# Optimization experiments

Hardware: AMD Instinct MI355X
Metric: run time of the kernel (lower is better)

## Reference

```python
import jax, jax.numpy as jnp
import numpy as np

LN_EPS = 1e-5
B, N, D, V = 2048, 8, 1024, 4096


def setup_inputs() -> dict:
    key = jax.random.key(0)
    k1, k2, k3, k4 = jax.random.split(key, 4)
    return {
        "input_embedding": jax.random.normal(k1, (B, D), dtype=jnp.float32),
        "features": jax.random.randint(k2, (B, N), 0, V, dtype=jnp.int64),
        "embed_tables": jax.random.normal(k3, (N, V, D), dtype=jnp.float32) * 0.02,
        "W_pred": jax.random.normal(k4, (N, D, V), dtype=jnp.float32) * 0.02,
        "b_pred": jnp.zeros((N, V), dtype=jnp.float32),
        "ln_gamma": jnp.ones((D,), dtype=jnp.float32),
        "ln_beta": jnp.zeros((D,), dtype=jnp.float32),
    }


def reference(input_embedding, features, embed_tables, W_pred, b_pred, ln_gamma, ln_beta):
    # Per-feature embedding lookup: embed_tables[n, features[b,n]] -> [B, N, D]
    feat_emb = embed_tables[jnp.arange(N)[None, :], features]
    # Stack input embedding in front: [B, N+1, D]
    embeddings = jnp.concatenate([input_embedding[:, None, :], feat_emb], axis=1)
    # Original: triu(diag=1) mask-multiply-sum then [:, 1:, :].
    # masked_sums[:, t] = sum_{s < t} emb[:, s]; slicing t=1..N == inclusive cumsum
    # over the first N positions.
    masked_sums = jnp.cumsum(embeddings, axis=1)[:, :-1, :]  # [B, N, D]
    # LayerNorm over last dim
    mu = jnp.mean(masked_sums, axis=-1, keepdims=True)
    var = jnp.var(masked_sums, axis=-1, keepdims=True)
    h = (masked_sums - mu) / jnp.sqrt(var + LN_EPS) * ln_gamma + ln_beta
    # Exact (erf) GELU, matching nn.GELU default
    h = jax.nn.gelu(h, approximate=False)
    # Per-feature predictor heads as one batched GEMM: [B, N, V]
    logits = jnp.einsum("bnd,ndv->bnv", h, W_pred) + b_pred
    return logits
```

## Files before the change

### kernel.cpp

```cpp
#include <hip/hip_runtime.h>
#include <hip/hip_bf16.h>

#define B_ 2048
#define N_ 8
#define D_ 1024
#define V_ 4096
#define LN_EPS_ 1e-5f

typedef __bf16 bf16x8 __attribute__((ext_vector_type(8)));
typedef float f32x4 __attribute__((ext_vector_type(4)));

#define GLB(p) ((const __attribute__((address_space(1))) void*)(p))
#define LDSP(p) ((__attribute__((address_space(3))) void*)(p))

static __device__ __forceinline__ unsigned short f2bf(float x) {
    union { float f; unsigned int u; } v;
    v.f = x;
    unsigned int r = v.u + 0x7fffu + ((v.u >> 16) & 1u);
    return (unsigned short)(r >> 16);
}

__global__ __launch_bounds__(256) void prep(const float* __restrict__ ie,
                                            const int* __restrict__ feats,
                                            const float* __restrict__ emb,
                                            const float* __restrict__ gamma,
                                            const float* __restrict__ beta,
                                            const float* __restrict__ W,
                                            unsigned short* __restrict__ H,
                                            unsigned short* __restrict__ Wt) {
    const int bid = blockIdx.x;
    const int t = threadIdx.x;

    if (bid >= 2048) {
        __shared__ unsigned short tile[64][65];
        const int w  = bid - 2048;
        const int v0 = (w & 63) * 64;
        const int d0 = ((w >> 6) & 15) * 64;
        const int n  = w >> 10;
        const int tx = t & 15, ty = t >> 4;
#pragma unroll
        for (int i = 0; i < 4; ++i) {
            const int d = ty + i * 16;
            const float4 w4 = *(const float4*)&W[((size_t)n * D_ + d0 + d) * V_ + v0 + tx * 4];
            tile[d][tx * 4 + 0] = f2bf(w4.x);
            tile[d][tx * 4 + 1] = f2bf(w4.y);
            tile[d][tx * 4 + 2] = f2bf(w4.z);
            tile[d][tx * 4 + 3] = f2bf(w4.w);
        }
        __syncthreads();
#pragma unroll
        for (int i = 0; i < 4; ++i) {
            const int v = ty + i * 16;
            ushort4 pk;
            pk.x = tile[tx * 4 + 0][v];
            pk.y = tile[tx * 4 + 1][v];
            pk.z = tile[tx * 4 + 2][v];
            pk.w = tile[tx * 4 + 3][v];
            *reinterpret_cast<ushort4*>(&Wt[((size_t)n * V_ + v0 + v) * D_ + d0 + tx * 4]) = pk;
        }
    } else {
        __shared__ float redS[4], redQ[4];
        const int b = bid;
        const int d0 = t * 4;
        const int lane = t & 63, wid = t >> 6;

        float4 s  = *(const float4*)&ie[(size_t)b * D_ + d0];
        const float4 g4 = *(const float4*)&gamma[d0];
        const float4 be4 = *(const float4*)&beta[d0];

        int fc[N_];
#pragma unroll
        for (int n = 0; n < N_; ++n) fc[n] = feats[b * N_ + n];

#pragma unroll
        for (int n = 0; n < N_; ++n) {
            float ls = s.x + s.y + s.z + s.w;
            float lq = s.x * s.x + s.y * s.y + s.z * s.z + s.w * s.w;
#pragma unroll
            for (int off = 32; off > 0; off >>= 1) {
                ls += __shfl_down(ls, off, 64);
                lq += __shfl_down(lq, off, 64);
            }
            if (lane == 0) { redS[wid] = ls; redQ[wid] = lq; }
            __syncthreads();
            const float tot  = redS[0] + redS[1] + redS[2] + redS[3];
            const float totq = redQ[0] + redQ[1] + redQ[2] + redQ[3];
            __syncthreads();

            const float mu   = tot * (1.0f / D_);
            const float var  = totq * (1.0f / D_) - mu * mu;
            const float rstd = rsqrtf(var + LN_EPS_);

            float h0 = (s.x - mu) * rstd * g4.x + be4.x;
            float h1 = (s.y - mu) * rstd * g4.y + be4.y;
            float h2 = (s.z - mu) * rstd * g4.z + be4.z;
            float h3 = (s.w - mu) * rstd * g4.w + be4.w;
            h0 = 0.5f * h0 * (1.0f + erff(h0 * 0.70710678f));
            h1 = 0.5f * h1 * (1.0f + erff(h1 * 0.70710678f));
            h2 = 0.5f * h2 * (1.0f + erff(h2 * 0.70710678f));
            h3 = 0.5f * h3 * (1.0f + erff(h3 * 0.70710678f));

            ushort4 pk;
            pk.x = f2bf(h0); pk.y = f2bf(h1); pk.z = f2bf(h2); pk.w = f2bf(h3);
            *reinterpret_cast<ushort4*>(&H[((size_t)n * B_ + b) * D_ + d0]) = pk;

            const float4 e = *(const float4*)&emb[((size_t)n * V_ + fc[n]) * (size_t)D_ + d0];
            s.x += e.x; s.y += e.y; s.z += e.z; s.w += e.w;
        }
    }
}

#define MF(a, b, c) __builtin_amdgcn_mfma_f32_16x16x32_bf16((a), (b), (c), 0, 0, 0)

#define STAGE(As, Bs, bb) { \
    __builtin_amdgcn_global_load_lds(GLB((As) + (size_t)srow * D_ + gsl),         LDSP(lds + (bb) + t * 16), 16, 0, 0); \
    __builtin_amdgcn_global_load_lds(GLB((As) + (size_t)(srow + 128) * D_ + gsl), LDSP(lds + (bb) + 8192 + t * 16), 16, 0, 0); \
    __builtin_amdgcn_global_load_lds(GLB((Bs) + (size_t)srow * D_ + gsl),         LDSP(lds + (bb) + 16384 + t * 16), 16, 0, 0); \
    __builtin_amdgcn_global_load_lds(GLB((Bs) + (size_t)(srow + 128) * D_ + gsl), LDSP(lds + (bb) + 24576 + t * 16), 16, 0, 0); \
}

#define RD_A(i, bb) (*(const bf16x8*)(lds + (bb) + ((i) * 32 + wr * 16 + lrow) * 64 + swk))
#define RD_B(j, bb) (*(const bf16x8*)(lds + (bb) + 16384 + (wc * 64 + (j) * 16 + lrow) * 64 + swk))

#define TILE1(bc, bn, As, Bs) { \
    asm volatile("s_waitcnt vmcnt(8)" ::: "memory"); \
    __builtin_amdgcn_s_barrier(); \
    STAGE(As, Bs, bn); \
    bf16x8 Bf[4], Af[4]; \
    _Pragma("unroll") for (int j = 0; j < 4; ++j) Bf[j] = RD_B(j, bc); \
    _Pragma("unroll") for (int i = 0; i < 4; ++i) Af[i] = RD_A(i, bc); \
    __builtin_amdgcn_s_setprio(1); \
    _Pragma("unroll") for (int i = 0; i < 4; ++i) \
        _Pragma("unroll") for (int j = 0; j < 4; ++j) \
            acc[i][j] = MF(Af[i], Bf[j], acc[i][j]); \
    __builtin_amdgcn_s_setprio(0); \
    _Pragma("unroll") for (int i = 0; i < 4; ++i) Af[i] = RD_A((i) + 4, bc); \
    __builtin_amdgcn_s_setprio(1); \
    _Pragma("unroll") for (int i = 0; i < 4; ++i) \
        _Pragma("unroll") for (int j = 0; j < 4; ++j) \
            acc[i + 4][j] = MF(Af[i], Bf[j], acc[i + 4][j]); \
    __builtin_amdgcn_s_setprio(0); \
}

__global__ __launch_bounds__(512, 2) void gemm4(const unsigned short* __restrict__ H,
                                                const unsigned short* __restrict__ Wt,
                                                const float* __restrict__ bp,
                                                float* __restrict__ out) {
    extern __shared__ char lds[];
    const int bid = blockIdx.x;
    const int logical = (bid & 7) * 128 + (bid >> 3);
    const int n  = logical >> 7;
    const int mt = (logical >> 4) & 7;
    const int vt = logical & 15;

    const int t = threadIdx.x;
    const int wid = t >> 6, lane = t & 63;
    const int wr = wid >> 2, wc = wid & 3;

    const unsigned short* Ab = H  + ((size_t)n * B_ + (size_t)mt * 256) * D_;
    const unsigned short* Bb = Wt + ((size_t)n * V_ + (size_t)vt * 256) * D_;

    const int srow = t >> 2;
    const int gsl  = ((t & 3) ^ (srow & 3)) * 8;
    const int lrow = lane & 15;
    const int swk  = (((lane >> 4) ^ (lrow & 3))) * 16;
    const int col  = lane & 15;
    const int rg   = (lane >> 4) * 4;

    float bias[4];
#pragma unroll
    for (int j = 0; j < 4; ++j)
        bias[j] = bp[(size_t)n * V_ + vt * 256 + wc * 64 + j * 16 + col];
    __builtin_amdgcn_sched_barrier(0);

    f32x4 acc[8][4] = {};

    STAGE(Ab, Bb, 0);
    STAGE(Ab + 32, Bb + 32, 32768);
    STAGE(Ab + 64, Bb + 64, 65536);

#pragma unroll 1
    for (int it = 0; it < 8; ++it) {
        const int k0 = it * 128;
        const int s0 = k0 + 96;
        int s1 = k0 + 128; if (s1 >= 1024) s1 = 0;
        int s2 = k0 + 160; if (s2 >= 1024) s2 = 0;
        int s3 = k0 + 192; if (s3 >= 1024) s3 = 0;
        TILE1(0,     98304, Ab + s0, Bb + s0);
        TILE1(32768, 0,     Ab + s1, Bb + s1);
        TILE1(65536, 32768, Ab + s2, Bb + s2);
        TILE1(98304, 65536, Ab + s3, Bb + s3);
    }
    asm volatile("s_waitcnt vmcnt(0)" ::: "memory");

    const int gc0 = vt * 256 + wc * 64 + col;
#pragma unroll
    for (int i = 0; i < 8; ++i) {
        const int row = mt * 256 + i * 32 + wr * 16 + rg;
#pragma unroll
        for (int j = 0; j < 4; ++j) {
            const int gcol = gc0 + j * 16;
#pragma unroll
            for (int r = 0; r < 4; ++r)
                out[((size_t)(row + r) * N_ + n) * V_ + gcol] = acc[i][j][r] + bias[j];
        }
    }
}

extern "C" void kernel_launch(void* const* d_in, const int* in_sizes, int n_in,
                              void* d_out, int out_size, void* d_ws, size_t ws_size,
                              hipStream_t stream) {
    const float* ie  = (const float*)d_in[0];
    const int*   fts = (const int*)d_in[1];
    const float* emb = (const float*)d_in[2];
    const float* W   = (const float*)d_in[3];
    const float* bp  = (const float*)d_in[4];
    const float* gam = (const float*)d_in[5];
    const float* bet = (const float*)d_in[6];
    float* out = (float*)d_out;

    unsigned short* Wt = (unsigned short*)d_ws;
    unsigned short* H  = (unsigned short*)((char*)d_ws + (size_t)N_ * V_ * D_ * 2);

    (void)hipFuncSetAttribute(reinterpret_cast<const void*>(gemm4),
                              hipFuncAttributeMaxDynamicSharedMemorySize, 131072);

    prep<<<dim3(2048 + 8192), dim3(256), 0, stream>>>(ie, fts, emb, gam, bet, W, H, Wt);
    gemm4<<<dim3(1024), dim3(512), 131072, stream>>>(H, Wt, bp, out);
}
```

Baseline: 244.4 us.

## Make GEMM persistent across heads with 256x128 tiles and triple-buffered K64 stages

Replaces the one-tile-per-block batched GEMM (1024 blocks, 256x256 tiles, K32 stages) with 256 blocks. Each block loops over all 8 heads for a fixed 256x128 output tile, running a continuous K64 triple-buffered pipeline that prefetches across head boundaries and writes each head's epilogue inline. The aim is to remove per-block prologue and epilogue pipeline drain and launch tail, and to halve the barrier count through larger K steps. The costs are a smaller N tile with lower arithmetic intensity, only 256 blocks on the GPU, and 144KB LDS per block, which may limit occupancy to one block per CU.

Result: no change. 243.9 us (-0.2%).

```diff
diff --git a/kernel.cpp b/kernel.cpp
--- a/kernel.cpp
+++ b/kernel.cpp
@@ -110,100 +110,140 @@
     }
 }
 
+#define BUFSZ 49152
+
 #define MF(a, b, c) __builtin_amdgcn_mfma_f32_16x16x32_bf16((a), (b), (c), 0, 0, 0)
 
-#define STAGE(As, Bs, bb) { \
-    __builtin_amdgcn_global_load_lds(GLB((As) + (size_t)srow * D_ + gsl),         LDSP(lds + (bb) + t * 16), 16, 0, 0); \
-    __builtin_amdgcn_global_load_lds(GLB((As) + (size_t)(srow + 128) * D_ + gsl), LDSP(lds + (bb) + 8192 + t * 16), 16, 0, 0); \
-    __builtin_amdgcn_global_load_lds(GLB((Bs) + (size_t)srow * D_ + gsl),         LDSP(lds + (bb) + 16384 + t * 16), 16, 0, 0); \
-    __builtin_amdgcn_global_load_lds(GLB((Bs) + (size_t)(srow + 128) * D_ + gsl), LDSP(lds + (bb) + 24576 + t * 16), 16, 0, 0); \
-}
-
-#define RD_A(i, bb) (*(const bf16x8*)(lds + (bb) + ((i) * 32 + wr * 16 + lrow) * 64 + swk))
-#define RD_B(j, bb) (*(const bf16x8*)(lds + (bb) + 16384 + (wc * 64 + (j) * 16 + lrow) * 64 + swk))
-
-#define TILE1(bc, bn, As, Bs) { \
-    asm volatile("s_waitcnt vmcnt(8)" ::: "memory"); \
+#define STAGE6(As, Bs, bb) { \
+    __builtin_amdgcn_global_load_lds(GLB((As) + (size_t)(srow      ) * D_ + gsl), LDSP(lds + (bb) +          t * 16), 16, 0, 0); \
+    __builtin_amdgcn_global_load_lds(GLB((As) + (size_t)(srow +  64) * D_ + gsl), LDSP(lds + (bb) +  8192 + t * 16), 16, 0, 0); \
+    __builtin_amdgcn_global_load_lds(GLB((As) + (size_t)(srow + 128) * D_ + gsl), LDSP(lds + (bb) + 16384 + t * 16), 16, 0, 0); \
+    __builtin_amdgcn_global_load_lds(GLB((As) + (size_t)(srow + 192) * D_ + gsl), LDSP(lds + (bb) + 24576 + t * 16), 16, 0, 0); \
+    __builtin_amdgcn_global_load_lds(GLB((Bs) + (size_t)(srow      ) * D_ + gsl), LDSP(lds + (bb) + 32768 + t * 16), 16, 0, 0); \
+    __builtin_amdgcn_global_load_lds(GLB((Bs) + (size_t)(srow +  64) * D_ + gsl), LDSP(lds + (bb) + 40960 + t * 16), 16, 0, 0); \
+}
+
+#define RD_A(i, ks, bb) (*(const bf16x8*)(lds + (bb) + \
+    (wr * 128 + (i) * 16 + lrow) * 128 + ((((ks) * 4 + lkq) ^ (lrow & 7)) * 16)))
+#define RD_B(j, ks, bb) (*(const bf16x8*)(lds + (bb) + 32768 + \
+    (wc * 32 + (j) * 16 + lrow) * 128 + ((((ks) * 4 + lkq) ^ (lrow & 7)) * 16)))
+
+#define MFI(i, Ak0, Ak1) \
+    acc[i][0] = MF(Ak0, B00, acc[i][0]); \
+    acc[i][0] = MF(Ak1, B01, acc[i][0]); \
+    acc[i][1] = MF(Ak0, B10, acc[i][1]); \
+    acc[i][1] = MF(Ak1, B11, acc[i][1]);
+
+#define COMPUTE(bb) { \
+    bf16x8 B00 = RD_B(0, 0, bb), B01 = RD_B(0, 1, bb), B10 = RD_B(1, 0, bb), B11 = RD_B(1, 1, bb); \
+    bf16x8 A00 = RD_A(0, 0, bb), A01 = RD_A(0, 1, bb), A10 = RD_A(1, 0, bb), A11 = RD_A(1, 1, bb); \
+    bf16x8 A20 = RD_A(2, 0, bb), A21 = RD_A(2, 1, bb), A30 = RD_A(3, 0, bb), A31 = RD_A(3, 1, bb); \
+    __builtin_amdgcn_s_setprio(1); \
+    MFI(0, A00, A01) MFI(1, A10, A11) MFI(2, A20, A21) MFI(3, A30, A31) \
+    __builtin_amdgcn_s_setprio(0); \
+    A00 = RD_A(4, 0, bb); A01 = RD_A(4, 1, bb); A10 = RD_A(5, 0, bb); A11 = RD_A(5, 1, bb); \
+    A20 = RD_A(6, 0, bb); A21 = RD_A(6, 1, bb); A30 = RD_A(7, 0, bb); A31 = RD_A(7, 1, bb); \
+    __builtin_amdgcn_s_setprio(1); \
+    MFI(4, A00, A01) MFI(5, A10, A11) MFI(6, A20, A21) MFI(7, A30, A31) \
+    __builtin_amdgcn_s_setprio(0); \
+}
+
+#define TILE_STEP(GS, bc, bn) { \
+    const int gs_ = (GS) & 127; \
+    const int n2_ = gs_ >> 4; \
+    const int k2_ = (gs_ & 15) * 64; \
+    const unsigned short* As = H  + ((size_t)n2_ * B_ + (size_t)mt * 256) * D_ + k2_; \
+    const unsigned short* Bs = Wt + ((size_t)n2_ * V_ + (size_t)vt * 128) * D_ + k2_; \
+    asm volatile("s_waitcnt vmcnt(6)" ::: "memory"); \
     __builtin_amdgcn_s_barrier(); \
-    STAGE(As, Bs, bn); \
-    bf16x8 Bf[4], Af[4]; \
-    _Pragma("unroll") for (int j = 0; j < 4; ++j) Bf[j] = RD_B(j, bc); \
-    _Pragma("unroll") for (int i = 0; i < 4; ++i) Af[i] = RD_A(i, bc); \
-    __builtin_amdgcn_s_setprio(1); \
-    _Pragma("unroll") for (int i = 0; i < 4; ++i) \
-        _Pragma("unroll") for (int j = 0; j < 4; ++j) \
-            acc[i][j] = MF(Af[i], Bf[j], acc[i][j]); \
-    __builtin_amdgcn_s_setprio(0); \
-    _Pragma("unroll") for (int i = 0; i < 4; ++i) Af[i] = RD_A((i) + 4, bc); \
-    __builtin_amdgcn_s_setprio(1); \
-    _Pragma("unroll") for (int i = 0; i < 4; ++i) \
-        _Pragma("unroll") for (int j = 0; j < 4; ++j) \
-            acc[i + 4][j] = MF(Af[i], Bf[j], acc[i + 4][j]); \
-    __builtin_amdgcn_s_setprio(0); \
-}
-
-__global__ __launch_bounds__(512, 2) void gemm4(const unsigned short* __restrict__ H,
+    STAGE6(As, Bs, bn); \
+    COMPUTE(bc); \
+}
+
+#define EPILOG(nn) { \
+    _Pragma("unroll") for (int i = 0; i < 8; ++i) { \
+        const int row = mt * 256 + wr * 128 + i * 16 + rg; \
+        _Pragma("unroll") for (int r = 0; r < 4; ++r) { \
+            float* po = out + ((size_t)(row + r) * N_ + (nn)) * V_ + gc0; \
+            po[0]  = acc[i][0][r] + bb0[nn]; \
+            po[16] = acc[i][1][r] + bb1[nn]; \
+        } \
+        acc[i][0] = (f32x4){0.f, 0.f, 0.f, 0.f}; \
+        acc[i][1] = (f32x4){0.f, 0.f, 0.f, 0.f}; \
+    } \
+}
+
+#define TILE_BND(nn, bc, bn) { \
+    asm volatile("s_waitcnt vmcnt(6)" ::: "memory"); \
+    __builtin_amdgcn_s_barrier(); \
+    COMPUTE(bc); \
+    EPILOG(nn); \
+    __builtin_amdgcn_sched_barrier(0); \
+    { \
+        const int gs_ = ((nn) * 16 + 17) & 127; \
+        const int n2_ = gs_ >> 4; \
+        const int k2_ = (gs_ & 15) * 64; \
+        const unsigned short* As = H  + ((size_t)n2_ * B_ + (size_t)mt * 256) * D_ + k2_; \
+        const unsigned short* Bs = Wt + ((size_t)n2_ * V_ + (size_t)vt * 128) * D_ + k2_; \
+        STAGE6(As, Bs, bn); \
+    } \
+    asm volatile("s_waitcnt vmcnt(6)" ::: "memory"); \
+}
+
+__global__ __launch_bounds__(512, 2) void gemmd(const unsigned short* __restrict__ H,
                                                 const unsigned short* __restrict__ Wt,
                                                 const float* __restrict__ bp,
                                                 float* __restrict__ out) {
     extern __shared__ char lds[];
     const int bid = blockIdx.x;
-    const int logical = (bid & 7) * 128 + (bid >> 3);
-    const int n  = logical >> 7;
-    const int mt = (logical >> 4) & 7;
-    const int vt = logical & 15;
+    const int logical = (bid & 7) * 32 + (bid >> 3);
+    const int vt = (logical >> 5) * 4 + (logical & 3);
+    const int mt = (logical >> 2) & 7;
 
     const int t = threadIdx.x;
     const int wid = t >> 6, lane = t & 63;
-    const int wr = wid >> 2, wc = wid & 3;
-
-    const unsigned short* Ab = H  + ((size_t)n * B_ + (size_t)mt * 256) * D_;
-    const unsigned short* Bb = Wt + ((size_t)n * V_ + (size_t)vt * 256) * D_;
-
-    const int srow = t >> 2;
-    const int gsl  = ((t & 3) ^ (srow & 3)) * 8;
+    const int wr = wid >> 2;
+    const int wc = wid & 3;
+
+    const int srow = t >> 3;
+    const int gsl  = ((t & 7) ^ ((t >> 3) & 7)) * 8;
     const int lrow = lane & 15;
-    const int swk  = (((lane >> 4) ^ (lrow & 3))) * 16;
+    const int lkq  = lane >> 4;
     const int col  = lane & 15;
     const int rg   = (lane >> 4) * 4;
-
-    float bias[4];
-#pragma unroll
-    for (int j = 0; j < 4; ++j)
-        bias[j] = bp[(size_t)n * V_ + vt * 256 + wc * 64 + j * 16 + col];
-    __builtin_amdgcn_sched_barrier(0);
-
-    f32x4 acc[8][4] = {};
-
-    STAGE(Ab, Bb, 0);
-    STAGE(Ab + 32, Bb + 32, 32768);
-    STAGE(Ab + 64, Bb + 64, 65536);
-
+    const int gc0  = vt * 128 + wc * 32 + col;
+
+    float bb0[8], bb1[8];
+#pragma unroll
+    for (int n = 0; n < 8; ++n) {
+        bb0[n] = bp[(size_t)n * V_ + gc0];
+        bb1[n] = bp[(size_t)n * V_ + gc0 + 16];
+    }
+    asm volatile("s_waitcnt vmcnt(0)" ::: "memory");
+
+    f32x4 acc[8][2] = {};
+
+    {
+        const unsigned short* As = H  + (size_t)mt * 256 * D_;
+        const unsigned short* Bs = Wt + (size_t)vt * 128 * D_;
+        STAGE6(As, Bs, 0);
+        STAGE6(As + 64, Bs + 64, BUFSZ);
+    }
+
+#pragma unroll
+    for (int n = 0; n < 8; ++n) {
+        constexpr int P0 = 0, P1 = BUFSZ, P2 = 2 * BUFSZ;
+        const int c0 = (n % 3 == 0) ? P0 : (n % 3 == 1) ? P1 : P2;
+        const int c1 = (n % 3 == 0) ? P1 : (n % 3 == 1) ? P2 : P0;
+        const int c2 = (n % 3 == 0) ? P2 : (n % 3 == 1) ? P0 : P1;
 #pragma unroll 1
-    for (int it = 0; it < 8; ++it) {
-        const int k0 = it * 128;
-        const int s0 = k0 + 96;
-        int s1 = k0 + 128; if (s1 >= 1024) s1 = 0;
-        int s2 = k0 + 160; if (s2 >= 1024) s2 = 0;
-        int s3 = k0 + 192; if (s3 >= 1024) s3 = 0;
-        TILE1(0,     98304, Ab + s0, Bb + s0);
-        TILE1(32768, 0,     Ab + s1, Bb + s1);
-        TILE1(65536, 32768, Ab + s2, Bb + s2);
-        TILE1(98304, 65536, Ab + s3, Bb + s3);
-    }
-    asm volatile("s_waitcnt vmcnt(0)" ::: "memory");
-
-    const int gc0 = vt * 256 + wc * 64 + col;
-#pragma unroll
-    for (int i = 0; i < 8; ++i) {
-        const int row = mt * 256 + i * 32 + wr * 16 + rg;
-#pragma unroll
-        for (int j = 0; j < 4; ++j) {
-            const int gcol = gc0 + j * 16;
-#pragma unroll
-            for (int r = 0; r < 4; ++r)
-                out[((size_t)(row + r) * N_ + n) * V_ + gcol] = acc[i][j][r] + bias[j];
-        }
+        for (int kk5 = 0; kk5 < 5; ++kk5) {
+            const int g0 = n * 16 + kk5 * 3;
+            TILE_STEP(g0 + 2, c0, c2);
+            TILE_STEP(g0 + 3, c1, c0);
+            TILE_STEP(g0 + 4, c2, c1);
+        }
+        TILE_BND(n, c0, c2);
     }
 }
 
@@ -222,9 +262,9 @@
     unsigned short* Wt = (unsigned short*)d_ws;
     unsigned short* H  = (unsigned short*)((char*)d_ws + (size_t)N_ * V_ * D_ * 2);
 
-    (void)hipFuncSetAttribute(reinterpret_cast<const void*>(gemm4),
-                              hipFuncAttributeMaxDynamicSharedMemorySize, 131072);
+    (void)hipFuncSetAttribute(reinterpret_cast<const void*>(gemmd),
+                              hipFuncAttributeMaxDynamicSharedMemorySize, 3 * BUFSZ);
 
     prep<<<dim3(2048 + 8192), dim3(256), 0, stream>>>(ie, fts, emb, gam, bet, W, H, Wt);
-    gemm4<<<dim3(1024), dim3(512), 131072, stream>>>(H, Wt, bp, out);
-}
+    gemmd<<<dim3(256), dim3(512), 3 * BUFSZ, stream>>>(H, Wt, bp, out);
+}
```

## Rewrite GEMM as persistent 256-block kernel with 32x32 MFMA and register-staged loads

Applied to the files above, without the earlier changes.

The GEMM is restructured so each of 256 blocks walks four consecutive V tiles for one (n, M tile), with the epilogue writing and zeroing accumulators between tiles. Tiles are now loaded through registers and written to double-buffered swizzled LDS instead of direct global-to-LDS loads with four-stage buffering, and the math uses 32x32x16 bf16 MFMA. The goal is to cut launch and tail overhead, reuse the A tile address stream, and lower LDS read traffic per FLOP. In exchange, the grid is only 256 blocks (one wave of occupancy), pipelining depth is reduced, and every step waits on vmcnt(0).

Measured after the change: 300.6 us. 23.0% more time.

```diff
diff --git a/kernel.cpp b/kernel.cpp
--- a/kernel.cpp
+++ b/kernel.cpp
@@ -8,10 +8,7 @@
 #define LN_EPS_ 1e-5f
 
 typedef __bf16 bf16x8 __attribute__((ext_vector_type(8)));
-typedef float f32x4 __attribute__((ext_vector_type(4)));
-
-#define GLB(p) ((const __attribute__((address_space(1))) void*)(p))
-#define LDSP(p) ((__attribute__((address_space(3))) void*)(p))
+typedef float f32x16 __attribute__((ext_vector_type(16)));
 
 static __device__ __forceinline__ unsigned short f2bf(float x) {
     union { float f; unsigned int u; } v;
@@ -110,101 +107,132 @@
     }
 }
 
-#define MF(a, b, c) __builtin_amdgcn_mfma_f32_16x16x32_bf16((a), (b), (c), 0, 0, 0)
-
-#define STAGE(As, Bs, bb) { \
-    __builtin_amdgcn_global_load_lds(GLB((As) + (size_t)srow * D_ + gsl),         LDSP(lds + (bb) + t * 16), 16, 0, 0); \
-    __builtin_amdgcn_global_load_lds(GLB((As) + (size_t)(srow + 128) * D_ + gsl), LDSP(lds + (bb) + 8192 + t * 16), 16, 0, 0); \
-    __builtin_amdgcn_global_load_lds(GLB((Bs) + (size_t)srow * D_ + gsl),         LDSP(lds + (bb) + 16384 + t * 16), 16, 0, 0); \
-    __builtin_amdgcn_global_load_lds(GLB((Bs) + (size_t)(srow + 128) * D_ + gsl), LDSP(lds + (bb) + 24576 + t * 16), 16, 0, 0); \
-}
-
-#define RD_A(i, bb) (*(const bf16x8*)(lds + (bb) + ((i) * 32 + wr * 16 + lrow) * 64 + swk))
-#define RD_B(j, bb) (*(const bf16x8*)(lds + (bb) + 16384 + (wc * 64 + (j) * 16 + lrow) * 64 + swk))
-
-#define TILE1(bc, bn, As, Bs) { \
-    asm volatile("s_waitcnt vmcnt(8)" ::: "memory"); \
+#define MF32(a, b, c) __builtin_amdgcn_mfma_f32_32x32x16_bf16((a), (b), (c), 0, 0, 0)
+
+#define GLOADS(G2) { \
+    const unsigned short* pa = Abase + ((G2) & 15) * 64; \
+    const unsigned short* pb = Bb0 + (size_t)((G2) >> 4) * (256 * D_) + ((G2) & 15) * 64; \
+    ra0 = *(const float4*)(pa); \
+    ra1 = *(const float4*)(pa +  64 * D_); \
+    ra2 = *(const float4*)(pa + 128 * D_); \
+    ra3 = *(const float4*)(pa + 192 * D_); \
+    rb0 = *(const float4*)(pb); \
+    rb1 = *(const float4*)(pb +  64 * D_); \
+    rb2 = *(const float4*)(pb + 128 * D_); \
+    rb3 = *(const float4*)(pb + 192 * D_); \
+}
+
+#define DSWRITES(BN) { \
+    char* wp = lds + (BN) + wby; \
+    *(float4*)(wp)         = ra0; \
+    *(float4*)(wp + 1024)  = ra1; \
+    *(float4*)(wp + 2048)  = ra2; \
+    *(float4*)(wp + 3072)  = ra3; \
+    *(float4*)(wp + 32768) = rb0; \
+    *(float4*)(wp + 33792) = rb1; \
+    *(float4*)(wp + 34816) = rb2; \
+    *(float4*)(wp + 35840) = rb3; \
+}
+
+#define COMPUTE(BC) { \
+    _Pragma("unroll") for (int kk = 0; kk < 4; ++kk) { \
+        const char* rp = lds + (BC); \
+        bf16x8 b0 = *(const bf16x8*)(rp + CBb[kk]); \
+        bf16x8 b1 = *(const bf16x8*)(rp + CBb[kk] + 512); \
+        bf16x8 a0 = *(const bf16x8*)(rp + CAb[kk]); \
+        bf16x8 a1 = *(const bf16x8*)(rp + CAb[kk] + 512); \
+        bf16x8 a2 = *(const bf16x8*)(rp + CAb[kk] + 1024); \
+        bf16x8 a3 = *(const bf16x8*)(rp + CAb[kk] + 1536); \
+        __builtin_amdgcn_s_setprio(1); \
+        acc[0][0] = MF32(a0, b0, acc[0][0]); acc[0][1] = MF32(a0, b1, acc[0][1]); \
+        acc[1][0] = MF32(a1, b0, acc[1][0]); acc[1][1] = MF32(a1, b1, acc[1][1]); \
+        acc[2][0] = MF32(a2, b0, acc[2][0]); acc[2][1] = MF32(a2, b1, acc[2][1]); \
+        acc[3][0] = MF32(a3, b0, acc[3][0]); acc[3][1] = MF32(a3, b1, acc[3][1]); \
+        __builtin_amdgcn_s_setprio(0); \
+    } \
+}
+
+#define STEP(BC, BN, G, DO_W, DO_I) { \
+    asm volatile("s_waitcnt lgkmcnt(0)" ::: "memory"); \
     __builtin_amdgcn_s_barrier(); \
-    STAGE(As, Bs, bn); \
-    bf16x8 Bf[4], Af[4]; \
-    _Pragma("unroll") for (int j = 0; j < 4; ++j) Bf[j] = RD_B(j, bc); \
-    _Pragma("unroll") for (int i = 0; i < 4; ++i) Af[i] = RD_A(i, bc); \
-    __builtin_amdgcn_s_setprio(1); \
-    _Pragma("unroll") for (int i = 0; i < 4; ++i) \
-        _Pragma("unroll") for (int j = 0; j < 4; ++j) \
-            acc[i][j] = MF(Af[i], Bf[j], acc[i][j]); \
-    __builtin_amdgcn_s_setprio(0); \
-    _Pragma("unroll") for (int i = 0; i < 4; ++i) Af[i] = RD_A((i) + 4, bc); \
-    __builtin_amdgcn_s_setprio(1); \
-    _Pragma("unroll") for (int i = 0; i < 4; ++i) \
-        _Pragma("unroll") for (int j = 0; j < 4; ++j) \
-            acc[i + 4][j] = MF(Af[i], Bf[j], acc[i + 4][j]); \
-    __builtin_amdgcn_s_setprio(0); \
-}
-
-__global__ __launch_bounds__(512, 2) void gemm4(const unsigned short* __restrict__ H,
+    asm volatile("s_waitcnt vmcnt(0)" ::: "memory"); \
+    if (DO_W) DSWRITES(BN); \
+    if (DO_I) GLOADS((G) + 2); \
+    COMPUTE(BC); \
+}
+
+#define EPILOG(JB, ZERO) { \
+    const int vt_ = vtg * 4 + (JB); \
+    const int gcb = vt_ * 256 + wc * 64 + l31; \
+    const float bj0 = bp[(size_t)n * V_ + gcb]; \
+    const float bj1 = bp[(size_t)n * V_ + gcb + 32]; \
+    _Pragma("unroll") for (int i = 0; i < 4; ++i) { \
+        _Pragma("unroll") for (int r = 0; r < 16; ++r) { \
+            const int row = mt * 256 + wr * 128 + i * 32 + (r & 3) + 8 * (r >> 2) + 4 * h; \
+            float* po = out + (size_t)row * (N_ * V_) + (size_t)n * V_ + gcb; \
+            po[0]  = acc[i][0][r] + bj0; \
+            po[32] = acc[i][1][r] + bj1; \
+        } \
+        if (ZERO) { \
+            _Pragma("unroll") for (int r = 0; r < 16; ++r) { acc[i][0][r] = 0.f; acc[i][1][r] = 0.f; } \
+        } \
+    } \
+}
+
+__global__ __launch_bounds__(512, 2) void gemmp(const unsigned short* __restrict__ H,
                                                 const unsigned short* __restrict__ Wt,
                                                 const float* __restrict__ bp,
                                                 float* __restrict__ out) {
     extern __shared__ char lds[];
     const int bid = blockIdx.x;
-    const int logical = (bid & 7) * 128 + (bid >> 3);
-    const int n  = logical >> 7;
-    const int mt = (logical >> 4) & 7;
-    const int vt = logical & 15;
+    const int n   = bid & 7;
+    const int c   = bid >> 3;
+    const int mt  = c & 7;
+    const int vtg = c >> 3;
 
     const int t = threadIdx.x;
     const int wid = t >> 6, lane = t & 63;
     const int wr = wid >> 2, wc = wid & 3;
-
-    const unsigned short* Ab = H  + ((size_t)n * B_ + (size_t)mt * 256) * D_;
-    const unsigned short* Bb = Wt + ((size_t)n * V_ + (size_t)vt * 256) * D_;
-
-    const int srow = t >> 2;
-    const int gsl  = ((t & 3) ^ (srow & 3)) * 8;
-    const int lrow = lane & 15;
-    const int swk  = (((lane >> 4) ^ (lrow & 3))) * 16;
-    const int col  = lane & 15;
-    const int rg   = (lane >> 4) * 4;
-
-    float bias[4];
-#pragma unroll
-    for (int j = 0; j < 4; ++j)
-        bias[j] = bp[(size_t)n * V_ + vt * 256 + wc * 64 + j * 16 + col];
-    __builtin_amdgcn_sched_barrier(0);
-
-    f32x4 acc[8][4] = {};
-
-    STAGE(Ab, Bb, 0);
-    STAGE(Ab + 32, Bb + 32, 32768);
-    STAGE(Ab + 64, Bb + 64, 65536);
+    const int h = lane >> 5, l31 = lane & 31;
+
+    const int goff = (t >> 3) * D_ + (t & 7) * 8;
+    const int wby  = ((t & 7) * 256 + ((t >> 3) ^ (((t & 7) & 3) << 3))) * 16;
+
+    int CAb[4], CBb[4];
+#pragma unroll
+    for (int kk = 0; kk < 4; ++kk) {
+        const int sA = 2 * kk + h;
+        const int lx = l31 ^ ((sA & 3) << 3);
+        CAb[kk] = (sA * 256 + wr * 128 + lx) * 16;
+        CBb[kk] = (sA * 256 + wc * 64 + lx) * 16 + 32768;
+    }
+
+    const unsigned short* Abase = H  + ((size_t)n * B_ + (size_t)mt * 256) * D_ + goff;
+    const unsigned short* Bb0   = Wt + ((size_t)n * V_ + (size_t)vtg * 1024) * D_ + goff;
+
+    f32x16 acc[4][2];
+#pragma unroll
+    for (int i = 0; i < 4; ++i)
+#pragma unroll
+        for (int r = 0; r < 16; ++r) { acc[i][0][r] = 0.f; acc[i][1][r] = 0.f; }
+
+    float4 ra0, ra1, ra2, ra3, rb0, rb1, rb2, rb3;
+
+    GLOADS(0);
+    asm volatile("s_waitcnt vmcnt(0)" ::: "memory");
+    DSWRITES(0);
+    GLOADS(1);
 
 #pragma unroll 1
-    for (int it = 0; it < 8; ++it) {
-        const int k0 = it * 128;
-        const int s0 = k0 + 96;
-        int s1 = k0 + 128; if (s1 >= 1024) s1 = 0;
-        int s2 = k0 + 160; if (s2 >= 1024) s2 = 0;
-        int s3 = k0 + 192; if (s3 >= 1024) s3 = 0;
-        TILE1(0,     98304, Ab + s0, Bb + s0);
-        TILE1(32768, 0,     Ab + s1, Bb + s1);
-        TILE1(65536, 32768, Ab + s2, Bb + s2);
-        TILE1(98304, 65536, Ab + s3, Bb + s3);
+    for (int gp = 0; gp < 31; ++gp) {
+        const int g = gp * 2;
+        STEP(0,     65536, g,     1, 1);
+        STEP(65536, 0,     g + 1, 1, 1);
+        if ((gp & 7) == 7) { EPILOG(gp >> 3, 1); }
     }
-    asm volatile("s_waitcnt vmcnt(0)" ::: "memory");
-
-    const int gc0 = vt * 256 + wc * 64 + col;
-#pragma unroll
-    for (int i = 0; i < 8; ++i) {
-        const int row = mt * 256 + i * 32 + wr * 16 + rg;
-#pragma unroll
-        for (int j = 0; j < 4; ++j) {
-            const int gcol = gc0 + j * 16;
-#pragma unroll
-            for (int r = 0; r < 4; ++r)
-                out[((size_t)(row + r) * N_ + n) * V_ + gcol] = acc[i][j][r] + bias[j];
-        }
-    }
+    STEP(0,     65536, 62, 1, 0);
+    STEP(65536, 0,     63, 0, 0);
+    EPILOG(3, 0);
 }
 
 extern "C" void kernel_launch(void* const* d_in, const int* in_sizes, int n_in,
@@ -222,9 +250,9 @@
     unsigned short* Wt = (unsigned short*)d_ws;
     unsigned short* H  = (unsigned short*)((char*)d_ws + (size_t)N_ * V_ * D_ * 2);
 
-    (void)hipFuncSetAttribute(reinterpret_cast<const void*>(gemm4),
+    (void)hipFuncSetAttribute(reinterpret_cast<const void*>(gemmp),
                               hipFuncAttributeMaxDynamicSharedMemorySize, 131072);
 
     prep<<<dim3(2048 + 8192), dim3(256), 0, stream>>>(ie, fts, emb, gam, bet, W, H, Wt);
-    gemm4<<<dim3(1024), dim3(512), 131072, stream>>>(H, Wt, bp, out);
-}
+    gemmp<<<dim3(256), dim3(512), 131072, stream>>>(H, Wt, bp, out);
+}
```

## Restructure GEMM LDS pipeline: prefetch depth two, issue loads after fragment reads, new swizzle

Applied to the files above, without the earlier changes.

Changes the 4-buffer LDS ring so that, for each k-step, the fragment reads from the current buffer are issued first. Only then are async global->LDS loads for two steps ahead issued, followed by a wait and barrier, and a second barrier at the end of each tile. It removes the wrap-around redundant loads (the old loop staged k=0 again at the end), peels the final tiles, and changes the XOR swizzle to use different row bits. The aim is to reduce LDS bank conflicts and avoid wasted loads. The cost is an extra barrier per tile and a shallower prefetch.

Measured after the change: 240.9 us. Within noise of the previous version (-1.4%).

```diff
diff --git a/kernel.cpp b/kernel.cpp
--- a/kernel.cpp
+++ b/kernel.cpp
@@ -112,37 +112,38 @@
 
 #define MF(a, b, c) __builtin_amdgcn_mfma_f32_16x16x32_bf16((a), (b), (c), 0, 0, 0)
 
-#define STAGE(As, Bs, bb) { \
-    __builtin_amdgcn_global_load_lds(GLB((As) + (size_t)srow * D_ + gsl),         LDSP(lds + (bb) + t * 16), 16, 0, 0); \
-    __builtin_amdgcn_global_load_lds(GLB((As) + (size_t)(srow + 128) * D_ + gsl), LDSP(lds + (bb) + 8192 + t * 16), 16, 0, 0); \
-    __builtin_amdgcn_global_load_lds(GLB((Bs) + (size_t)srow * D_ + gsl),         LDSP(lds + (bb) + 16384 + t * 16), 16, 0, 0); \
-    __builtin_amdgcn_global_load_lds(GLB((Bs) + (size_t)(srow + 128) * D_ + gsl), LDSP(lds + (bb) + 24576 + t * 16), 16, 0, 0); \
-}
-
-#define RD_A(i, bb) (*(const bf16x8*)(lds + (bb) + ((i) * 32 + wr * 16 + lrow) * 64 + swk))
-#define RD_B(j, bb) (*(const bf16x8*)(lds + (bb) + 16384 + (wc * 64 + (j) * 16 + lrow) * 64 + swk))
-
-#define TILE1(bc, bn, As, Bs) { \
-    asm volatile("s_waitcnt vmcnt(8)" ::: "memory"); \
+#define STAGE2(KS, bb) { \
+    __builtin_amdgcn_global_load_lds(GLB(Ab + (KS) + (size_t)(srow      ) * D_ + gsl), LDSP(lds + (bb) +         t * 16), 16, 0, 0); \
+    __builtin_amdgcn_global_load_lds(GLB(Ab + (KS) + (size_t)(srow + 128) * D_ + gsl), LDSP(lds + (bb) +  8192 + t * 16), 16, 0, 0); \
+    __builtin_amdgcn_global_load_lds(GLB(Bb + (KS) + (size_t)(srow      ) * D_ + gsl), LDSP(lds + (bb) + 16384 + t * 16), 16, 0, 0); \
+    __builtin_amdgcn_global_load_lds(GLB(Bb + (KS) + (size_t)(srow + 128) * D_ + gsl), LDSP(lds + (bb) + 24576 + t * 16), 16, 0, 0); \
+}
+
+#define RD_A2(i, bb) (*(const bf16x8*)(lds + (bb) + ((i) * 32 + wr * 16 + lrow) * 64 + swk))
+#define RD_B2(j, bb) (*(const bf16x8*)(lds + (bb) + 16384 + (wc * 64 + (j) * 16 + lrow) * 64 + swk))
+
+#define TILE2(bc, bn, KS, VM, DOSTG) { \
+    bf16x8 Bf[4], Af[4]; \
+    _Pragma("unroll") for (int j = 0; j < 4; ++j) Bf[j] = RD_B2(j, bc); \
+    _Pragma("unroll") for (int i = 0; i < 4; ++i) Af[i] = RD_A2(i, bc); \
+    if (DOSTG) { STAGE2(KS, bn); } \
+    asm volatile("s_waitcnt vmcnt(" #VM ")" ::: "memory"); \
     __builtin_amdgcn_s_barrier(); \
-    STAGE(As, Bs, bn); \
-    bf16x8 Bf[4], Af[4]; \
-    _Pragma("unroll") for (int j = 0; j < 4; ++j) Bf[j] = RD_B(j, bc); \
-    _Pragma("unroll") for (int i = 0; i < 4; ++i) Af[i] = RD_A(i, bc); \
     __builtin_amdgcn_s_setprio(1); \
     _Pragma("unroll") for (int i = 0; i < 4; ++i) \
         _Pragma("unroll") for (int j = 0; j < 4; ++j) \
             acc[i][j] = MF(Af[i], Bf[j], acc[i][j]); \
     __builtin_amdgcn_s_setprio(0); \
-    _Pragma("unroll") for (int i = 0; i < 4; ++i) Af[i] = RD_A((i) + 4, bc); \
+    _Pragma("unroll") for (int i = 0; i < 4; ++i) Af[i] = RD_A2((i) + 4, bc); \
     __builtin_amdgcn_s_setprio(1); \
     _Pragma("unroll") for (int i = 0; i < 4; ++i) \
         _Pragma("unroll") for (int j = 0; j < 4; ++j) \
             acc[i + 4][j] = MF(Af[i], Bf[j], acc[i + 4][j]); \
     __builtin_amdgcn_s_setprio(0); \
-}
-
-__global__ __launch_bounds__(512, 2) void gemm4(const unsigned short* __restrict__ H,
+    __builtin_amdgcn_s_barrier(); \
+}
+
+__global__ __launch_bounds__(512, 2) void gemm2(const unsigned short* __restrict__ H,
                                                 const unsigned short* __restrict__ Wt,
                                                 const float* __restrict__ bp,
                                                 float* __restrict__ out) {
@@ -161,9 +162,10 @@
     const unsigned short* Bb = Wt + ((size_t)n * V_ + (size_t)vt * 256) * D_;
 
     const int srow = t >> 2;
-    const int gsl  = ((t & 3) ^ (srow & 3)) * 8;
+    const int gsl  = ((t & 3) ^ ((t >> 3) & 3)) * 8;
     const int lrow = lane & 15;
-    const int swk  = (((lane >> 4) ^ (lrow & 3))) * 16;
+    const int lkq  = lane >> 4;
+    const int swk  = (lkq ^ ((lrow >> 1) & 3)) * 16;
     const int col  = lane & 15;
     const int rg   = (lane >> 4) * 4;
 
@@ -171,27 +173,28 @@
 #pragma unroll
     for (int j = 0; j < 4; ++j)
         bias[j] = bp[(size_t)n * V_ + vt * 256 + wc * 64 + j * 16 + col];
+    asm volatile("s_waitcnt vmcnt(0)" ::: "memory");
     __builtin_amdgcn_sched_barrier(0);
 
     f32x4 acc[8][4] = {};
 
-    STAGE(Ab, Bb, 0);
-    STAGE(Ab + 32, Bb + 32, 32768);
-    STAGE(Ab + 64, Bb + 64, 65536);
+    STAGE2(0, 0);
+    STAGE2(32, 32768);
+    asm volatile("s_waitcnt vmcnt(4)" ::: "memory");
+    __builtin_amdgcn_s_barrier();
 
 #pragma unroll 1
-    for (int it = 0; it < 8; ++it) {
-        const int k0 = it * 128;
-        const int s0 = k0 + 96;
-        int s1 = k0 + 128; if (s1 >= 1024) s1 = 0;
-        int s2 = k0 + 160; if (s2 >= 1024) s2 = 0;
-        int s3 = k0 + 192; if (s3 >= 1024) s3 = 0;
-        TILE1(0,     98304, Ab + s0, Bb + s0);
-        TILE1(32768, 0,     Ab + s1, Bb + s1);
-        TILE1(65536, 32768, Ab + s2, Bb + s2);
-        TILE1(98304, 65536, Ab + s3, Bb + s3);
+    for (int it = 0; it < 7; ++it) {
+        const int ks = it * 128 + 64;
+        TILE2(0,     65536, ks,      4, 1);
+        TILE2(32768, 98304, ks + 32, 4, 1);
+        TILE2(65536, 0,     ks + 64, 4, 1);
+        TILE2(98304, 32768, ks + 96, 4, 1);
     }
-    asm volatile("s_waitcnt vmcnt(0)" ::: "memory");
+    TILE2(0,     65536, 960, 4, 1);
+    TILE2(32768, 98304, 992, 4, 1);
+    TILE2(65536, 0,     0,   0, 0);
+    TILE2(98304, 0,     0,   0, 0);
 
     const int gc0 = vt * 256 + wc * 64 + col;
 #pragma unroll
@@ -222,9 +225,9 @@
     unsigned short* Wt = (unsigned short*)d_ws;
     unsigned short* H  = (unsigned short*)((char*)d_ws + (size_t)N_ * V_ * D_ * 2);
 
-    (void)hipFuncSetAttribute(reinterpret_cast<const void*>(gemm4),
+    (void)hipFuncSetAttribute(reinterpret_cast<const void*>(gemm2),
                               hipFuncAttributeMaxDynamicSharedMemorySize, 131072);
 
     prep<<<dim3(2048 + 8192), dim3(256), 0, stream>>>(ie, fts, emb, gam, bet, W, H, Wt);
-    gemm4<<<dim3(1024), dim3(512), 131072, stream>>>(H, Wt, bp, out);
-}
+    gemm2<<<dim3(1024), dim3(512), 131072, stream>>>(H, Wt, bp, out);
+}
```
